# Kernel optimization log

Hardware: AMD Instinct MI355X
Metric: run time of the kernel (lower is better)

The kernel has to match this reference:

```python
import jax, jax.numpy as jnp
import numpy as np

EMBED_DIM = 1024
NUM_HEADS = 16
HEAD_DIM = 64
B, S = 4, 2048


def setup_inputs() -> dict:
    key = jax.random.key(0)
    ks = jax.random.split(key, 5)
    std = 0.02
    x = jax.random.normal(ks[0], (B, S, EMBED_DIM), dtype=jnp.float32)
    Wq = std * jax.random.normal(ks[1], (NUM_HEADS, EMBED_DIM, HEAD_DIM), dtype=jnp.float32)
    Wk = std * jax.random.normal(ks[2], (NUM_HEADS, EMBED_DIM, HEAD_DIM), dtype=jnp.float32)
    Wv = std * jax.random.normal(ks[3], (NUM_HEADS, EMBED_DIM, HEAD_DIM), dtype=jnp.float32)
    Wo = std * jax.random.normal(ks[4], (NUM_HEADS, HEAD_DIM, EMBED_DIM), dtype=jnp.float32)
    bq = jnp.zeros((NUM_HEADS, HEAD_DIM), dtype=jnp.float32)
    bk = jnp.zeros((NUM_HEADS, HEAD_DIM), dtype=jnp.float32)
    bv = jnp.zeros((NUM_HEADS, HEAD_DIM), dtype=jnp.float32)
    bo = jnp.zeros((EMBED_DIM,), dtype=jnp.float32)
    return {"x": x, "Wq": Wq, "bq": bq, "Wk": Wk, "bk": bk,
            "Wv": Wv, "bv": bv, "Wo": Wo, "bo": bo}


def reference(x, Wq, bq, Wk, bk, Wv, bv, Wo, bo):
    # q,k,v: [b, s, n, h]
    q = jnp.einsum('bsd,ndh->bsnh', x, Wq) + bq
    k = jnp.einsum('bsd,ndh->bsnh', x, Wk) + bk
    v = jnp.einsum('bsd,ndh->bsnh', x, Wv) + bv
    scale = 1.0 / (HEAD_DIM ** 0.5)
    # non-causal full attention matrix [b, n, s, t]
    attn = jnp.einsum('bsnh,btnh->bnst', q, k) * scale
    attn = jax.nn.softmax(attn, axis=-1)
    after = jnp.einsum('bnst,btnh->bsnh', attn, v)
    out = jnp.einsum('bsnh,nhd->bsd', after, Wo) + bo
    return out
```

## Files before the change

kernel.cpp:

```cpp
#include <hip/hip_runtime.h>

typedef __bf16 bf16;
typedef bf16 bf16x8 __attribute__((ext_vector_type(8)));
typedef bf16 bf16x4 __attribute__((ext_vector_type(4)));
typedef bf16 bf16x2 __attribute__((ext_vector_type(2)));
typedef float f32x4 __attribute__((ext_vector_type(4)));
typedef float f32x16 __attribute__((ext_vector_type(16)));
typedef unsigned int u32;
typedef u32 u32x4 __attribute__((ext_vector_type(4)));

constexpr int Bb = 4, Ss = 2048, Dd = 1024, NH = 16, HD = 64;
constexpr int BS = Bb * Ss;
constexpr float CSC = 0.18033688011112042f;

__device__ __forceinline__ int sw(int row, int col) {
  return (row << 6) + (col ^ ((row & 7) << 3));
}

__device__ __forceinline__ void g2l16(const bf16* g, bf16* l) {
  __builtin_amdgcn_global_load_lds(
      (const __attribute__((address_space(1))) void*)g,
      (__attribute__((address_space(3))) void*)l, 16, 0, 0);
}

__device__ __forceinline__ u32 pkbf(float a, float b) {
  bf16x2 v = {(bf16)a, (bf16)b};
  return __builtin_bit_cast(u32, v);
}

__global__ void prep(const float* __restrict__ x, bf16* __restrict__ xb,
                     const float* __restrict__ Wq, const float* __restrict__ Wk,
                     const float* __restrict__ Wv, const float* __restrict__ Wo,
                     const float* __restrict__ bq, const float* __restrict__ bk,
                     const float* __restrict__ bv,
                     bf16* __restrict__ WT_all, bf16* __restrict__ WoT,
                     float* __restrict__ bias_all) {
  __shared__ bf16 Ts[64 * 72];
  const int t = threadIdx.x;
  if (blockIdx.y == 0) {
    int o = (blockIdx.x * 256 + t) * 4;
    f32x4 v = *(const f32x4*)&x[o];
    bf16x4 r = {(bf16)v[0], (bf16)v[1], (bf16)v[2], (bf16)v[3]};
    *(bf16x4*)&xb[o] = r;
    return;
  }
  if (blockIdx.x > 1024) return;
  if (blockIdx.x == 1024) {
    for (int j = t; j < 3072; j += 256) {
      int s2 = j >> 10;
      const float* bb = (s2 == 0) ? bq : (s2 == 1) ? bk : bv;
      bias_all[j] = bb[j & 1023] * (s2 == 0 ? CSC : 1.0f);
    }
    return;
  }
  const int sel = blockIdx.x >> 8, bx = blockIdx.x & 255;
  if (sel < 3) {
    const float* W = (sel == 0) ? Wq : (sel == 1) ? Wk : Wv;
    float scale = (sel == 0) ? CSC : 1.0f;
    int head = bx >> 4, dt = bx & 15;
    const float* src = W + head * 65536 + dt * 64 * 64;
#pragma unroll
    for (int i = 0; i < 4; ++i) {
      int idx = i * 256 + t;
      int dr = idx >> 4, hc = (idx & 15) * 4;
      f32x4 v = *(const f32x4*)&src[dr * 64 + hc];
#pragma unroll
      for (int k = 0; k < 4; ++k) Ts[(hc + k) * 72 + dr] = (bf16)(v[k] * scale);
    }
    __syncthreads();
    bf16* dst = WT_all + (size_t)sel * 1048576 + (size_t)(head * 64) * 1024 + dt * 64;
#pragma unroll
    for (int i = 0; i < 2; ++i) {
      int idx = i * 256 + t;
      int hr = idx >> 3, ch = (idx & 7) * 8;
      *(bf16x8*)&dst[(size_t)hr * 1024 + ch] = *(const bf16x8*)&Ts[hr * 72 + ch];
    }
  } else {
    int ct = bx >> 4, dt = bx & 15;
    const float* src = Wo + (size_t)(ct * 64) * 1024 + dt * 64;
#pragma unroll
    for (int i = 0; i < 4; ++i) {
      int idx = i * 256 + t;
      int cr = idx >> 4, dc = (idx & 15) * 4;
      f32x4 v = *(const f32x4*)&src[(size_t)cr * 1024 + dc];
#pragma unroll
      for (int k = 0; k < 4; ++k) Ts[(dc + k) * 72 + cr] = (bf16)v[k];
    }
    __syncthreads();
    bf16* dst = WoT + (size_t)(dt * 64) * 1024 + ct * 64;
#pragma unroll
    for (int i = 0; i < 2; ++i) {
      int idx = i * 256 + t;
      int dr = idx >> 3, ch = (idx & 7) * 8;
      *(bf16x8*)&dst[(size_t)dr * 1024 + ch] = *(const bf16x8*)&Ts[dr * 72 + ch];
    }
  }
}

__device__ __forceinline__ void gemm_core(const bf16* __restrict__ A,
                                          const bf16* __restrict__ BT,
                                          int m0, int n0, bf16* As, bf16* Bs,
                                          f32x4 (&acc)[4][4]) {
  const int t = threadIdx.x;
  const int l = t & 63, q = l >> 4, lm = l & 15;
  const int w = t >> 6, wm = w & 1, wn = w >> 1;
  int ro[4], co[4];
#pragma unroll
  for (int i = 0; i < 4; ++i) {
    int o = i * 256 + t;
    ro[i] = o >> 3;
    co[i] = ((o & 7) ^ ((o >> 3) & 7)) << 3;
  }
  const int lbase = (t & 192) * 8;
  for (int k0 = 0; k0 < 1024; k0 += 64) {
    __syncthreads();
#pragma unroll
    for (int i = 0; i < 4; ++i)
      g2l16(&A[(size_t)(m0 + ro[i]) * 1024 + k0 + co[i]], &As[i * 2048 + lbase]);
#pragma unroll
    for (int i = 0; i < 4; ++i)
      g2l16(&BT[(size_t)(n0 + ro[i]) * 1024 + k0 + co[i]], &Bs[i * 2048 + lbase]);
    __syncthreads();
#pragma unroll
    for (int kh = 0; kh < 2; ++kh) {
      bf16x8 a[4], b[4];
#pragma unroll
      for (int i = 0; i < 4; ++i)
        a[i] = *(const bf16x8*)&As[sw(wm * 64 + i * 16 + lm, kh * 32 + q * 8)];
#pragma unroll
      for (int i = 0; i < 4; ++i)
        b[i] = *(const bf16x8*)&Bs[sw(wn * 64 + i * 16 + lm, kh * 32 + q * 8)];
#pragma unroll
      for (int mt = 0; mt < 4; ++mt)
#pragma unroll
        for (int nt = 0; nt < 4; ++nt)
          acc[mt][nt] = __builtin_amdgcn_mfma_f32_16x16x32_bf16(a[mt], b[nt], acc[mt][nt], 0, 0, 0);
    }
  }
}

__global__ __launch_bounds__(256) void gemm_qkv(const bf16* __restrict__ xb,
                                                const bf16* __restrict__ WT,
                                                const float* __restrict__ bias_all,
                                                bf16* __restrict__ QKb,
                                                bf16* __restrict__ VTb) {
  __shared__ __align__(16) bf16 As[128 * 64];
  __shared__ __align__(16) bf16 Bs[128 * 64];
  const int bid = blockIdx.x;
  const int t = threadIdx.x;
  const int l = t & 63, q = l >> 4, lm = l & 15;
  const int w = t >> 6, wm = w & 1, wn = w >> 1;
  const bool vmode = bid >= 1024;
  int m0, n0;
  const bf16 *A, *BT;
  if (!vmode) {
    int xcd = bid & 7, idx = bid >> 3;
    m0 = (idx >> 1) * 128;
    n0 = (xcd * 2 + (idx & 1)) * 128;
    A = xb; BT = WT;
  } else {
    int b2 = bid - 1024;
    int xcd = b2 & 7, idx = b2 >> 3;
    m0 = (idx >> 3) * 128;
    n0 = (xcd * 8 + (idx & 7)) * 128;
    A = WT + (size_t)2048 * 1024; BT = xb;
  }
  f32x4 acc[4][4] = {};
  gemm_core(A, BT, m0, n0, As, Bs, acc);
  if (vmode) {
#pragma unroll
    for (int nt = 0; nt < 4; ++nt) {
      int sg = n0 + wn * 64 + nt * 16 + lm;
      size_t sb = (size_t)(sg >> 11) * 2097152 + (sg & 2047);
#pragma unroll
      for (int mt = 0; mt < 4; ++mt)
#pragma unroll
        for (int r = 0; r < 4; ++r) {
          int m = m0 + wm * 64 + mt * 16 + q * 4 + r;
          VTb[sb + (size_t)(m >> 6) * 131072 + (size_t)(m & 63) * 2048] =
              (bf16)(acc[mt][nt][r] + bias_all[2048 + m]);
        }
    }
  } else {
#pragma unroll
    for (int nt = 0; nt < 4; ++nt) {
      int col = n0 + wn * 64 + nt * 16 + lm;
      float bb = bias_all[col];
#pragma unroll
      for (int mt = 0; mt < 4; ++mt) {
        int row = m0 + wm * 64 + mt * 16 + q * 4;
#pragma unroll
        for (int r = 0; r < 4; ++r)
          QKb[(size_t)(row + r) * 2048 + col] = (bf16)(acc[mt][nt][r] + bb);
      }
    }
  }
}

__global__ __launch_bounds__(256) void gemm_out(const bf16* __restrict__ after,
                                                const bf16* __restrict__ WoT,
                                                const float* __restrict__ bo,
                                                float* __restrict__ out) {
  __shared__ __align__(16) bf16 As[128 * 64];
  __shared__ __align__(16) bf16 Bs[128 * 64];
  const int bid = blockIdx.x;
  const int t = threadIdx.x;
  const int l = t & 63, q = l >> 4, lm = l & 15;
  const int w = t >> 6, wm = w & 1, wn = w >> 1;
  const int xcd = bid & 7, idx = bid >> 3;
  const int n0 = xcd * 128, m0 = idx * 128;
  f32x4 acc[4][4] = {};
  gemm_core(after, WoT, m0, n0, As, Bs, acc);
#pragma unroll
  for (int nt = 0; nt < 4; ++nt) {
    int col = n0 + wn * 64 + nt * 16 + lm;
    float bb = bo[col];
#pragma unroll
    for (int mt = 0; mt < 4; ++mt) {
      int row = m0 + wm * 64 + mt * 16 + q * 4;
#pragma unroll
      for (int r = 0; r < 4; ++r)
        out[(size_t)(row + r) * 1024 + col] = acc[mt][nt][r] + bb;
    }
  }
}

__global__ __launch_bounds__(256, 4) void attn(const bf16* __restrict__ QK,
                                               const bf16* __restrict__ VT,
                                               bf16* __restrict__ after) {
  __shared__ __align__(16) bf16 Ks[2][64 * 64];
  __shared__ __align__(16) bf16 Vs[2][64 * 64];
  const int t = threadIdx.x;
  const int l = t & 63, w = t >> 6;
  const int lh = l & 31, H = l >> 5;
  const int f = blockIdx.x;
  const int bn = (f & 7) | ((f >> 7) << 3);
  const int s0 = ((f >> 3) & 15) * 128;
  const int b = bn >> 4, n = bn & 15;
  const bf16* Qb = QK + (size_t)(b * 2048) * 2048 + n * 64;
  const bf16* Kb = Qb + 1024;
  const bf16* Vtb = VT + (size_t)bn * 131072;
  int ro[4], co[4];
#pragma unroll
  for (int i = 0; i < 4; ++i) {
    int o = i * 256 + t;
    ro[i] = o >> 3;
    co[i] = ((o & 7) ^ ((o >> 3) & 7)) << 3;
  }
  const int lbase = (t & 192) * 8;
  bf16* Kflat = &Ks[0][0];
#pragma unroll
  for (int i = 0; i < 4; ++i)
    g2l16(&Qb[(size_t)(s0 + ro[i]) * 2048 + co[i]], Kflat + i * 2048 + lbase);
  __syncthreads();
  bf16x8 qb[4];
#pragma unroll
  for (int ks = 0; ks < 4; ++ks)
    qb[ks] = *(const bf16x8*)&Kflat[sw(w * 32 + lh, ks * 16 + H * 8)];
  __syncthreads();
#pragma unroll
  for (int i = 0; i < 2; ++i) {
    g2l16(&Kb[(size_t)ro[i] * 2048 + co[i]], &Ks[0][i * 2048 + lbase]);
    g2l16(&Vtb[(size_t)ro[i] * 2048 + co[i]], &Vs[0][i * 2048 + lbase]);
  }
  f32x16 o_acc[2] = {};
  float rs = 0.f;
  for (int rd = 0; rd < 32; ++rd) {
    const int cur = rd & 1;
    __syncthreads();
    if (rd < 31) {
      int t0n = (rd + 1) * 64, nb = cur ^ 1;
#pragma unroll
      for (int i = 0; i < 2; ++i) {
        g2l16(&Kb[(size_t)(t0n + ro[i]) * 2048 + co[i]], &Ks[nb][i * 2048 + lbase]);
        g2l16(&Vtb[(size_t)ro[i] * 2048 + t0n + co[i]], &Vs[nb][i * 2048 + lbase]);
      }
    }
#pragma unroll
    for (int tt = 0; tt < 2; ++tt) {
      f32x16 sc = {};
#pragma unroll
      for (int ks = 0; ks < 4; ++ks) {
        bf16x8 kb = *(const bf16x8*)&Ks[cur][sw(tt * 32 + lh, ks * 16 + H * 8)];
        sc = __builtin_amdgcn_mfma_f32_32x32x16_bf16(kb, qb[ks], sc, 0, 0, 0);
      }
      u32 pk[8], xx[8];
#pragma unroll
      for (int i = 0; i < 8; ++i) {
        float p0 = __builtin_amdgcn_exp2f(sc[2 * i]);
        float p1 = __builtin_amdgcn_exp2f(sc[2 * i + 1]);
        rs += p0 + p1;
        pk[i] = pkbf(p0, p1);
      }
#pragma unroll
      for (int i = 0; i < 8; ++i) xx[i] = __shfl_xor((int)pk[i], 32);
#pragma unroll
      for (int ks2 = 0; ks2 < 2; ++ks2) {
        u32x4 av;
        av[0] = H ? xx[ks2 * 4 + 2] : pk[ks2 * 4 + 0];
        av[1] = H ? xx[ks2 * 4 + 3] : pk[ks2 * 4 + 1];
        av[2] = H ? pk[ks2 * 4 + 2] : xx[ks2 * 4 + 0];
        av[3] = H ? pk[ks2 * 4 + 3] : xx[ks2 * 4 + 1];
        bf16x8 pa = __builtin_bit_cast(bf16x8, av);
#pragma unroll
        for (int ht = 0; ht < 2; ++ht) {
          bf16x8 vb = *(const bf16x8*)&Vs[cur][sw(ht * 32 + lh, tt * 32 + ks2 * 16 + H * 8)];
          o_acc[ht] = __builtin_amdgcn_mfma_f32_32x32x16_bf16(pa, vb, o_acc[ht], 0, 0, 0);
        }
      }
    }
  }
  rs += __shfl_xor(rs, 32);
  float inv = 1.f / rs;
#pragma unroll
  for (int r = 0; r < 16; ++r) {
    int sl = (r & 3) + 8 * (r >> 2) + 4 * H;
    float invr = __shfl(inv, sl);
    size_t base = (size_t)(b * 2048 + s0 + w * 32 + sl) * 1024 + n * 64;
#pragma unroll
    for (int ht = 0; ht < 2; ++ht)
      after[base + ht * 32 + lh] = (bf16)(o_acc[ht][r] * invr);
  }
}

extern "C" void kernel_launch(void* const* d_in, const int* in_sizes, int n_in,
                              void* d_out, int out_size, void* d_ws, size_t ws_size,
                              hipStream_t stream) {
  const float* x  = (const float*)d_in[0];
  const float* Wq = (const float*)d_in[1];
  const float* bq = (const float*)d_in[2];
  const float* Wk = (const float*)d_in[3];
  const float* bk = (const float*)d_in[4];
  const float* Wv = (const float*)d_in[5];
  const float* bv = (const float*)d_in[6];
  const float* Wo = (const float*)d_in[7];
  const float* bo = (const float*)d_in[8];
  float* out = (float*)d_out;

  bf16* WT_all    = (bf16*)d_ws;
  bf16* WoT       = WT_all + (size_t)3072 * 1024;
  float* bias_all = (float*)(WoT + (size_t)1024 * 1024);
  bf16* xb        = (bf16*)(bias_all + 4096);
  bf16* QKb       = xb + (size_t)BS * Dd;
  bf16* VTb       = QKb + (size_t)BS * 2048;
  bf16* after     = VTb + (size_t)Bb * NH * HD * Ss;

  prep<<<dim3(8192, 2), dim3(256), 0, stream>>>(x, xb, Wq, Wk, Wv, Wo, bq, bk, bv,
                                                WT_all, WoT, bias_all);
  gemm_qkv<<<dim3(1536), dim3(256), 0, stream>>>(xb, WT_all, bias_all, QKb, VTb);
  attn<<<dim3(1024), dim3(256), 0, stream>>>(QKb, VTb, after);
  gemm_out<<<dim3(512), dim3(256), 0, stream>>>(after, WoT, bo, out);
}
```

Before: 285.6 us.

## Stage V-transpose epilogue through LDS and use permlane32 swap in attention

The V-projection epilogue used to write scattered 2-byte transposed stores to global memory. It now stages the tile in swizzled shared memory and writes it out as coalesced 16-byte rows. In the attention kernel, the eight shfl_xor exchanges of packed probabilities are replaced by permlane32_swap when that builtin is available, which avoids the ds_bpermute traffic and the per-lane selects. The staging step adds two barriers and extra LDS writes, and the swap path relies on the builtin's lane semantics matching the old select logic.

```diff
diff --git a/kernel.cpp b/kernel.cpp
--- a/kernel.cpp
+++ b/kernel.cpp
@@ -8,6 +8,7 @@
 typedef float f32x16 __attribute__((ext_vector_type(16)));
 typedef unsigned int u32;
 typedef u32 u32x4 __attribute__((ext_vector_type(4)));
+typedef int i32x2 __attribute__((ext_vector_type(2)));
 
 constexpr int Bb = 4, Ss = 2048, Dd = 1024, NH = 16, HD = 64;
 constexpr int BS = Bb * Ss;
@@ -15,6 +16,9 @@
 
 __device__ __forceinline__ int sw(int row, int col) {
   return (row << 6) + (col ^ ((row & 7) << 3));
+}
+__device__ __forceinline__ int sw128(int row, int col) {
+  return (row << 7) + (col ^ ((row & 7) << 3));
 }
 
 __device__ __forceinline__ void g2l16(const bf16* g, bf16* l) {
@@ -144,8 +148,9 @@
                                                 const float* __restrict__ bias_all,
                                                 bf16* __restrict__ QKb,
                                                 bf16* __restrict__ VTb) {
-  __shared__ __align__(16) bf16 As[128 * 64];
-  __shared__ __align__(16) bf16 Bs[128 * 64];
+  __shared__ __align__(16) bf16 SMEM[2 * 128 * 64];
+  bf16* As = SMEM;
+  bf16* Bs = SMEM + 128 * 64;
   const int bid = blockIdx.x;
   const int t = threadIdx.x;
   const int l = t & 63, q = l >> 4, lm = l & 15;
@@ -168,19 +173,26 @@
   f32x4 acc[4][4] = {};
   gemm_core(A, BT, m0, n0, As, Bs, acc);
   if (vmode) {
+    __syncthreads();
 #pragma unroll
     for (int nt = 0; nt < 4; ++nt) {
-      int sg = n0 + wn * 64 + nt * 16 + lm;
-      size_t sb = (size_t)(sg >> 11) * 2097152 + (sg & 2047);
-#pragma unroll
-      for (int mt = 0; mt < 4; ++mt)
-#pragma unroll
-        for (int r = 0; r < 4; ++r) {
-          int m = m0 + wm * 64 + mt * 16 + q * 4 + r;
-          VTb[sb + (size_t)(m >> 6) * 131072 + (size_t)(m & 63) * 2048] =
-              (bf16)(acc[mt][nt][r] + bias_all[2048 + m]);
-        }
-    }
+      int sl = wn * 64 + nt * 16 + lm;
+#pragma unroll
+      for (int mt = 0; mt < 4; ++mt) {
+        int ml = wm * 64 + mt * 16 + q * 4;
+#pragma unroll
+        for (int r = 0; r < 4; ++r)
+          SMEM[sw128(ml + r, sl)] = (bf16)(acc[mt][nt][r] + bias_all[2048 + m0 + ml + r]);
+      }
+    }
+    __syncthreads();
+    int hh = t >> 1, half = (t & 1) * 64;
+    int m = m0 + hh;
+    size_t gb = (size_t)((n0 >> 11) * 16 + (m >> 6)) * 131072 +
+                (size_t)(m & 63) * 2048 + (n0 & 2047) + half;
+#pragma unroll
+    for (int k = 0; k < 8; ++k)
+      *(bf16x8*)&VTb[gb + k * 8] = *(const bf16x8*)&SMEM[sw128(hh, half + k * 8)];
   } else {
 #pragma unroll
     for (int nt = 0; nt < 4; ++nt) {
@@ -201,8 +213,7 @@
                                                 const bf16* __restrict__ WoT,
                                                 const float* __restrict__ bo,
                                                 float* __restrict__ out) {
-  __shared__ __align__(16) bf16 As[128 * 64];
-  __shared__ __align__(16) bf16 Bs[128 * 64];
+  __shared__ __align__(16) bf16 SMEM[2 * 128 * 64];
   const int bid = blockIdx.x;
   const int t = threadIdx.x;
   const int l = t & 63, q = l >> 4, lm = l & 15;
@@ -210,7 +221,7 @@
   const int xcd = bid & 7, idx = bid >> 3;
   const int n0 = xcd * 128, m0 = idx * 128;
   f32x4 acc[4][4] = {};
-  gemm_core(after, WoT, m0, n0, As, Bs, acc);
+  gemm_core(after, WoT, m0, n0, SMEM, SMEM + 128 * 64, acc);
 #pragma unroll
   for (int nt = 0; nt < 4; ++nt) {
     int col = n0 + wn * 64 + nt * 16 + lm;
@@ -284,7 +295,7 @@
         bf16x8 kb = *(const bf16x8*)&Ks[cur][sw(tt * 32 + lh, ks * 16 + H * 8)];
         sc = __builtin_amdgcn_mfma_f32_32x32x16_bf16(kb, qb[ks], sc, 0, 0, 0);
       }
-      u32 pk[8], xx[8];
+      u32 pk[8];
 #pragma unroll
       for (int i = 0; i < 8; ++i) {
         float p0 = __builtin_amdgcn_exp2f(sc[2 * i]);
@@ -293,14 +304,25 @@
         pk[i] = pkbf(p0, p1);
       }
 #pragma unroll
-      for (int i = 0; i < 8; ++i) xx[i] = __shfl_xor((int)pk[i], 32);
-#pragma unroll
       for (int ks2 = 0; ks2 < 2; ++ks2) {
         u32x4 av;
-        av[0] = H ? xx[ks2 * 4 + 2] : pk[ks2 * 4 + 0];
-        av[1] = H ? xx[ks2 * 4 + 3] : pk[ks2 * 4 + 1];
-        av[2] = H ? pk[ks2 * 4 + 2] : xx[ks2 * 4 + 0];
-        av[3] = H ? pk[ks2 * 4 + 3] : xx[ks2 * 4 + 1];
+#if __has_builtin(__builtin_amdgcn_permlane32_swap)
+        i32x2 sA = __builtin_amdgcn_permlane32_swap((int)pk[ks2 * 4 + 0], (int)pk[ks2 * 4 + 2],
+                                                    false, false);
+        i32x2 sB = __builtin_amdgcn_permlane32_swap((int)pk[ks2 * 4 + 1], (int)pk[ks2 * 4 + 3],
+                                                    false, false);
+        av[0] = (u32)sA[0]; av[1] = (u32)sB[0]; av[2] = (u32)sA[1]; av[3] = (u32)sB[1];
+#else
+        u32 xx[4];
+        xx[0] = __shfl_xor((int)pk[ks2 * 4 + 0], 32);
+        xx[1] = __shfl_xor((int)pk[ks2 * 4 + 1], 32);
+        xx[2] = __shfl_xor((int)pk[ks2 * 4 + 2], 32);
+        xx[3] = __shfl_xor((int)pk[ks2 * 4 + 3], 32);
+        av[0] = H ? xx[2] : pk[ks2 * 4 + 0];
+        av[1] = H ? xx[3] : pk[ks2 * 4 + 1];
+        av[2] = H ? pk[ks2 * 4 + 2] : xx[0];
+        av[3] = H ? pk[ks2 * 4 + 3] : xx[1];
+#endif
         bf16x8 pa = __builtin_bit_cast(bf16x8, av);
 #pragma unroll
         for (int ht = 0; ht < 2; ++ht) {
```

New measurement: 274.7 us. 1.04x faster.
